# Performance work log

Measured on AMD Instinct MI355X. Metric: run time of the kernel, lower is better.

## Reference

```python
import jax, jax.numpy as jnp
import numpy as np

BN_EPS = 1e-3  # keras BatchNormalization default epsilon
NEG_INF = -1e30


def _masked_row_softmax(adjT):
    # tf.sparse.softmax semantics: softmax over NONZERO entries of each row;
    # implicit zeros stay exactly zero.
    mask = adjT != 0
    logits = jnp.where(mask, adjT, NEG_INF)
    p = jax.nn.softmax(logits, axis=-1)
    return jnp.where(mask, p, 0.0)


def _batch_norm(x, gamma, beta):
    # training-mode BN over all axes except channels
    mean = jnp.mean(x, axis=(0, 1), keepdims=True)
    var = jnp.var(x, axis=(0, 1), keepdims=True)
    return (x - mean) * jax.lax.rsqrt(var + BN_EPS) * gamma + beta


def setup_inputs() -> dict:
    key = jax.random.key(0)
    ks = jax.random.split(key, 4)
    B, N, F = 1, 8192, 128
    C0, C1 = 256, 128
    features = jax.random.normal(ks[0], (B, N, F), dtype=jnp.float32)
    adj = jax.random.randint(ks[1], (B, N, N), 0, 2, dtype=jnp.int32)
    kernel_1 = jax.random.normal(ks[2], (F, C0), dtype=jnp.float32) * (1.0 / np.sqrt(F))
    kernel_2 = jax.random.normal(ks[3], (C0, C1), dtype=jnp.float32) * (1.0 / np.sqrt(C0))
    return {
        "features": features,
        "adj": adj,
        "kernel_1": kernel_1,
        "bias_1": jnp.zeros((C0,), jnp.float32),
        "gamma_1": jnp.ones((C0,), jnp.float32),
        "beta_1": jnp.zeros((C0,), jnp.float32),
        "kernel_2": kernel_2,
        "bias_2": jnp.zeros((C1,), jnp.float32),
        "gamma_2": jnp.ones((C1,), jnp.float32),
        "beta_2": jnp.zeros((C1,), jnp.float32),
    }


def reference(features, adj, kernel_1, bias_1, gamma_1, beta_1,
              kernel_2, bias_2, gamma_2, beta_2):
    # fltr transposed: (B, Nr, Np), then sparse softmax over last dim
    adjT = jnp.transpose(adj.astype(jnp.float32), (0, 2, 1))
    w = _masked_row_softmax(adjT)                      # (B, Nr, Np)
    # people -> region aggregation + projection
    region = jnp.matmul(w, features)                   # (B, Nr, F)
    region = jnp.matmul(region, kernel_1) + bias_1     # (B, Nr, C0)
    region = _batch_norm(region, gamma_1, beta_1)
    # region -> people aggregation + projection
    people = jnp.matmul(jnp.transpose(w, (0, 2, 1)), region)  # (B, Np, C0)
    people = jnp.matmul(people, kernel_2) + bias_2             # (B, Np, C1)
    people = _batch_norm(people, gamma_2, beta_2)
    return people
```

## Files before the change

### kernel.cpp

```cpp
#include <hip/hip_runtime.h>
#include <stdint.h>

typedef unsigned int u32;
typedef unsigned short u16;
typedef __attribute__((ext_vector_type(8))) short short8;
typedef __attribute__((ext_vector_type(4))) float f32x4;

#define N8K 8192

__device__ __forceinline__ float b2f(u16 u) { return __uint_as_float(((u32)u) << 16); }
__device__ __forceinline__ u16 f2b(float f) {
  u32 i = __float_as_uint(f);
  i += 0x7FFFu + ((i >> 16) & 1u);
  return (u16)(i >> 16);
}
__device__ __forceinline__ u32 pk01(int x, int y) { return (u32)__mul24(x | (y << 16), 0x3F80); }
__device__ __forceinline__ u32 pkf(float a, float b) { return (u32)f2b(a) | ((u32)f2b(b) << 16); }

__device__ __forceinline__ int dvote(const u16* f16) {
  u16 u = f16[threadIdx.x * 2];
  int e = (u >> 7) & 0xFF;
  return __syncthreads_count((e >= 0x60 && e <= 0x9F) ? 1 : 0) >= 128;
}

__device__ __forceinline__ void gl_lds16(const void* g, void* l) {
  __builtin_amdgcn_global_load_lds(
      (const __attribute__((address_space(1))) u32*)g,
      (__attribute__((address_space(3))) u32*)l, 16, 0, 0);
}

#define MFMA_4x4(As_, Bs_, aoff_, boff_)                                         \
  {                                                                              \
    short8 afr[4], bfr[4];                                                       \
    _Pragma("unroll") for (int i_ = 0; i_ < 4; ++i_)                             \
      afr[i_] = *(const short8*)(As_ + aoff_[i_]);                               \
    _Pragma("unroll") for (int j_ = 0; j_ < 4; ++j_)                             \
      bfr[j_] = *(const short8*)(Bs_ + boff_[j_]);                               \
    _Pragma("unroll") for (int i_ = 0; i_ < 4; ++i_)                             \
      _Pragma("unroll") for (int j_ = 0; j_ < 4; ++j_)                           \
        acc[i_][j_] = __builtin_amdgcn_mfma_f32_16x16x32_bf16(                   \
            afr[i_], bfr[j_], acc[i_][j_], 0, 0, 0);                             \
  }

#define ZERO_ACC()                                                               \
  f32x4 acc[4][4];                                                               \
  {                                                                              \
    const f32x4 fz = {0.f, 0.f, 0.f, 0.f};                                       \
    _Pragma("unroll") for (int i_ = 0; i_ < 4; ++i_)                             \
      _Pragma("unroll") for (int j_ = 0; j_ < 4; ++j_) acc[i_][j_] = fz;         \
  }

__global__ void k_prep(const void* __restrict__ featv, const void* __restrict__ K1v,
                       const void* __restrict__ K2v,
                       const void* __restrict__ b1v, const void* __restrict__ g1v,
                       const void* __restrict__ be1v, const void* __restrict__ b2v,
                       const void* __restrict__ g2v, const void* __restrict__ be2v,
                       u16* __restrict__ Ft, u16* __restrict__ K1T, u16* __restrict__ K2T,
                       float* __restrict__ deg, float* __restrict__ par,
                       float* __restrict__ bn1s, float* __restrict__ bn1q,
                       float* __restrict__ bn2s, float* __restrict__ bn2q) {
  const int b = blockIdx.x, t = threadIdx.x;
  const int flag = dvote((const u16*)featv);
  if (b < 256) {
    __shared__ __align__(16) u16 Ls[32 * 136];
    const int pr = t >> 3, ck = t & 7;
    u16 v[16];
    if (flag) {
      const u16* s = (const u16*)featv + (size_t)(b * 32 + pr) * 128 + ck * 16;
      uint4 a = *(const uint4*)(s);
      uint4 bq = *(const uint4*)(s + 8);
      *(uint4*)&v[0] = a; *(uint4*)&v[8] = bq;
    } else {
      const float* s = (const float*)featv + (size_t)(b * 32 + pr) * 128 + ck * 16;
#pragma unroll
      for (int i = 0; i < 16; ++i) v[i] = f2b(s[i]);
    }
    *(uint4*)(Ls + pr * 136 + ck * 16) = *(uint4*)&v[0];
    *(uint4*)(Ls + pr * 136 + ck * 16 + 8) = *(uint4*)&v[8];
    __syncthreads();
    const int f = t >> 1, h16 = (t & 1) * 16;
    u32 w[8];
#pragma unroll
    for (int i = 0; i < 8; ++i) {
      u16 lo = Ls[(h16 + 2 * i) * 136 + f];
      u16 hi = Ls[(h16 + 2 * i + 1) * 136 + f];
      w[i] = (u32)lo | ((u32)hi << 16);
    }
    u16* d = Ft + (size_t)b * 4096 + f * 32 + h16;
    *(uint4*)(d) = *(uint4*)&w[0];
    *(uint4*)(d + 8) = *(uint4*)&w[4];
  } else if (b < 272) {
    int o = ((b - 256) * 256 + t) << 3;
    int k0 = o >> 13, c = (o >> 5) & 255, kk = o & 31;
    uint4 w;
    if (flag) {
      const u16* s = (const u16*)K1v + (size_t)(k0 * 32 + kk) * 256 + c;
      w.x = (u32)s[0]    | ((u32)s[256]  << 16);
      w.y = (u32)s[512]  | ((u32)s[768]  << 16);
      w.z = (u32)s[1024] | ((u32)s[1280] << 16);
      w.w = (u32)s[1536] | ((u32)s[1792] << 16);
    } else {
      const float* s = (const float*)K1v + (size_t)(k0 * 32 + kk) * 256 + c;
      w.x = pkf(s[0], s[256]); w.y = pkf(s[512], s[768]);
      w.z = pkf(s[1024], s[1280]); w.w = pkf(s[1536], s[1792]);
    }
    *(uint4*)(K1T + o) = w;
  } else if (b < 288) {
    int o = ((b - 272) * 256 + t) << 3;
    int k0 = o >> 12, c = (o >> 5) & 127, kk = o & 31;
    uint4 w;
    if (flag) {
      const u16* s = (const u16*)K2v + (size_t)(k0 * 32 + kk) * 128 + c;
      w.x = (u32)s[0]   | ((u32)s[128] << 16);
      w.y = (u32)s[256] | ((u32)s[384] << 16);
      w.z = (u32)s[512] | ((u32)s[640] << 16);
      w.w = (u32)s[768] | ((u32)s[896] << 16);
    } else {
      const float* s = (const float*)K2v + (size_t)(k0 * 32 + kk) * 128 + c;
      w.x = pkf(s[0], s[128]); w.y = pkf(s[256], s[384]);
      w.z = pkf(s[512], s[640]); w.w = pkf(s[768], s[896]);
    }
    *(uint4*)(K2T + o) = w;
  } else {
    if (t < 256) {
      par[t]       = flag ? b2f(((const u16*)b1v)[t])  : ((const float*)b1v)[t];
      par[256 + t] = flag ? b2f(((const u16*)g1v)[t])  : ((const float*)g1v)[t];
      par[512 + t] = flag ? b2f(((const u16*)be1v)[t]) : ((const float*)be1v)[t];
      bn1s[t] = 0.f; bn1q[t] = 0.f;
    }
    if (t < 128) {
      par[768 + t]  = flag ? b2f(((const u16*)b2v)[t])  : ((const float*)b2v)[t];
      par[896 + t]  = flag ? b2f(((const u16*)g2v)[t])  : ((const float*)g2v)[t];
      par[1024 + t] = flag ? b2f(((const u16*)be2v)[t]) : ((const float*)be2v)[t];
      bn2s[t] = 0.f; bn2q[t] = 0.f;
    }
    for (int i = t; i < N8K; i += 256) deg[i] = 0.f;
  }
}

__global__ __launch_bounds__(256, 2)
void k_gemm1(const int* __restrict__ adj, const u16* __restrict__ Ft,
             float* __restrict__ P1, float* __restrict__ deg, int ksteps) {
  __shared__ __align__(16) u16 As[128 * 32];
  __shared__ __align__(16) u16 Bs[128 * 32];
  __shared__ float degp[128];
  const int t = threadIdx.x, bx = blockIdx.x;
  const int nt = bx & 63, s = bx >> 6;
  const int n0 = nt << 7;
  const int lane = t & 63, wv = t >> 6;
  const int wm = (wv & 1) << 6, wn = (wv >> 1) << 6;
  const int fm = lane & 15, fq = lane >> 4;
  if (t < 128) degp[t] = 0.0f;
  ZERO_ACC();
  int aoff[4], boff[4];
#pragma unroll
  for (int i = 0; i < 4; ++i) aoff[i] = (wm + i * 16 + fm) * 32 + fq * 8;
#pragma unroll
  for (int j = 0; j < 4; ++j) {
    int n = wn + j * 16 + fm;
    boff[j] = n * 32 + ((fq * 8) ^ (((n >> 2) & 3) << 3));
  }
  const int rb = t & 31, kb = t >> 5;
  const int* gB = adj + ((size_t)s * ksteps * 32 + kb * 4) * N8K + n0 + rb * 4;
  const char* gA = (const char*)(Ft + (size_t)s * ksteps * 4096);
  char* lA = (char*)As + ((t >> 6) << 10);
  const int goff = t << 4;
  u16* lb = Bs + (rb * 4) * 32 + ((kb * 4) ^ ((rb & 3) << 3));
  int ds0 = 0, ds1 = 0, ds2 = 0, ds3 = 0;
  for (int ks = 0; ks < ksteps; ++ks) {
    __syncthreads();
    gl_lds16(gA + goff, lA);
    gl_lds16(gA + 4096 + goff, lA + 4096);
    int4 a0 = *(const int4*)(gB);
    int4 a1 = *(const int4*)(gB + N8K);
    int4 a2 = *(const int4*)(gB + 2 * N8K);
    int4 a3 = *(const int4*)(gB + 3 * N8K);
    gA += 8192;
    gB += 32 * N8K;
    ds0 += a0.x + a1.x + a2.x + a3.x;
    ds1 += a0.y + a1.y + a2.y + a3.y;
    ds2 += a0.z + a1.z + a2.z + a3.z;
    ds3 += a0.w + a1.w + a2.w + a3.w;
    uint2 w;
    w.x = pk01(a0.x, a1.x); w.y = pk01(a2.x, a3.x); *(uint2*)(lb) = w;
    w.x = pk01(a0.y, a1.y); w.y = pk01(a2.y, a3.y); *(uint2*)(lb + 32) = w;
    w.x = pk01(a0.z, a1.z); w.y = pk01(a2.z, a3.z); *(uint2*)(lb + 64) = w;
    w.x = pk01(a0.w, a1.w); w.y = pk01(a2.w, a3.w); *(uint2*)(lb + 96) = w;
    __syncthreads();
    MFMA_4x4(As, Bs, aoff, boff);
  }
  atomicAdd(&degp[rb * 4 + 0], (float)ds0);
  atomicAdd(&degp[rb * 4 + 1], (float)ds1);
  atomicAdd(&degp[rb * 4 + 2], (float)ds2);
  atomicAdd(&degp[rb * 4 + 3], (float)ds3);
  float* base = P1 + ((size_t)s * N8K + n0) * 128;
#pragma unroll
  for (int i = 0; i < 4; ++i)
#pragma unroll
    for (int j = 0; j < 4; ++j) {
      int r = wn + j * 16 + fm;
      int f = wm + i * 16 + fq * 4;
      *(f32x4*)(base + (size_t)r * 128 + f) = acc[i][j];
    }
  __syncthreads();
  if (t < 128) atomicAdd(&deg[n0 + t], degp[t]);
}

__global__ __launch_bounds__(256, 2)
void k_projf(const float* __restrict__ Psrc, const float* __restrict__ deg,
             const u16* __restrict__ Bt, const float* __restrict__ bias,
             float* __restrict__ Cout, float* __restrict__ bns, float* __restrict__ bnq,
             int nsplit, int ksteps, int Ncols, int useinv) {
  __shared__ __align__(16) u16 As[128 * 32];
  __shared__ __align__(16) u16 Bs[128 * 32];
  const int t = threadIdx.x, bx = blockIdx.x;
  const int ct = bx & 1, mt = (bx >> 1) & 63;
  const int m0 = mt << 7, n0 = ct << 7;
  const int lane = t & 63, wv = t >> 6;
  const int wm = (wv & 1) << 6, wn = (wv >> 1) << 6;
  const int fm = lane & 15, fq = lane >> 4;
  const int K = ksteps << 5;
  ZERO_ACC();
  int aoff[4], boff[4];
#pragma unroll
  for (int i = 0; i < 4; ++i) {
    int m = wm + i * 16 + fm;
    aoff[i] = m * 32 + ((fq * 8) ^ (((m >> 2) & 3) << 3));
  }
#pragma unroll
  for (int j = 0; j < 4; ++j) boff[j] = (wn + j * 16 + fm) * 32 + fq * 8;
  const int row = t >> 1;
  const size_t sstride = (size_t)N8K * K;
  const float* src = Psrc + (size_t)(m0 + row) * K + (t & 1) * 16;
  float inv = 1.0f;
  if (useinv) {
    float d = deg[m0 + row];
    inv = (d > 0.5f) ? 1.0f / d : 0.0f;
  }
  const int swzA = ((t >> 3) & 3) << 3;
  u16* la0 = As + row * 32 + (((t & 1) * 16) ^ swzA);
  u16* la1 = As + row * 32 + ((((t & 1) * 16) + 8) ^ swzA);
  char* lB = (char*)Bs + ((t >> 6) << 10);
  const int goff = t << 4;
  for (int ks = 0; ks < ksteps; ++ks) {
    __syncthreads();
    const char* gB = (const char*)(Bt + ((size_t)ks * Ncols + n0) * 32);
    gl_lds16(gB + goff, lB);
    gl_lds16(gB + 4096 + goff, lB + 4096);
    f32x4 s0 = {0.f, 0.f, 0.f, 0.f}, s1 = s0, s2 = s0, s3 = s0;
    const float* p = src + ks * 32;
    for (int sp = 0; sp < nsplit; ++sp) {
      const f32x4* q = (const f32x4*)(p + sp * sstride);
      s0 += q[0]; s1 += q[1]; s2 += q[2]; s3 += q[3];
    }
    s0 *= inv; s1 *= inv; s2 *= inv; s3 *= inv;
    uint4 w;
    w.x = pkf(s0[0], s0[1]); w.y = pkf(s0[2], s0[3]);
    w.z = pkf(s1[0], s1[1]); w.w = pkf(s1[2], s1[3]);
    *(uint4*)la0 = w;
    w.x = pkf(s2[0], s2[1]); w.y = pkf(s2[2], s2[3]);
    w.z = pkf(s3[0], s3[1]); w.w = pkf(s3[2], s3[3]);
    *(uint4*)la1 = w;
    __syncthreads();
    MFMA_4x4(As, Bs, aoff, boff);
  }
#pragma unroll
  for (int j = 0; j < 4; ++j) {
    int c = n0 + wn + j * 16 + fm;
    float bc = bias[c];
    float t1 = 0.f, t2 = 0.f;
#pragma unroll
    for (int i = 0; i < 4; ++i) {
      int r = m0 + wm + i * 16 + fq * 4;
#pragma unroll
      for (int ii = 0; ii < 4; ++ii) {
        float v = acc[i][j][ii] + bc;
        Cout[(size_t)(r + ii) * Ncols + c] = v;
        t1 += v; t2 += v * v;
      }
    }
    t1 += __shfl_xor(t1, 16); t1 += __shfl_xor(t1, 32);
    t2 += __shfl_xor(t2, 16); t2 += __shfl_xor(t2, 32);
    if (fq == 0) { atomicAdd(&bns[c], t1); atomicAdd(&bnq[c], t2); }
  }
}

__global__ __launch_bounds__(256, 2)
void k_bnH(const float* __restrict__ region1, const float* __restrict__ deg,
           const float* __restrict__ bn1s, const float* __restrict__ bn1q,
           const float* __restrict__ g1, const float* __restrict__ be1,
           const u16* __restrict__ K2T, u16* __restrict__ HT) {
  __shared__ __align__(16) u16 As[128 * 32];
  __shared__ __align__(16) u16 Bs[128 * 32];
  __shared__ float scS[256], shS[256];
  const int t = threadIdx.x, mt = blockIdx.x;
  const int m0 = mt << 7;
  const int lane = t & 63, wv = t >> 6;
  const int wm = (wv & 1) << 6, wn = (wv >> 1) << 6;
  const int fm = lane & 15, fq = lane >> 4;
  {
    float mu = bn1s[t] * (1.0f / 8192.0f);
    float var = bn1q[t] * (1.0f / 8192.0f) - mu * mu;
    float iv = rsqrtf(var + 1e-3f);
    float sc = iv * g1[t];
    scS[t] = sc;
    shS[t] = be1[t] - mu * sc;
  }
  ZERO_ACC();
  int aoff[4], boff[4];
#pragma unroll
  for (int i = 0; i < 4; ++i) {
    int m = wm + i * 16 + fm;
    aoff[i] = m * 32 + ((fq * 8) ^ (((m >> 2) & 3) << 3));
  }
#pragma unroll
  for (int j = 0; j < 4; ++j) boff[j] = (wn + j * 16 + fm) * 32 + fq * 8;
  const int row = t >> 1, half = t & 1;
  float d = deg[m0 + row];
  const float idg = (d > 0.5f) ? 1.0f / d : 0.0f;
  const float* src = region1 + (size_t)(m0 + row) * 256 + half * 16;
  const int swzA = ((t >> 3) & 3) << 3;
  u16* la0 = As + row * 32 + ((half * 16) ^ swzA);
  u16* la1 = As + row * 32 + (((half * 16) + 8) ^ swzA);
  char* lB = (char*)Bs + ((t >> 6) << 10);
  const int goff = t << 4;
  for (int ks = 0; ks < 8; ++ks) {
    __syncthreads();
    const char* gB = (const char*)(K2T + (size_t)ks * 4096);
    gl_lds16(gB + goff, lB);
    gl_lds16(gB + 4096 + goff, lB + 4096);
    const float* p = src + ks * 32;
    const int cb = ks * 32 + half * 16;
    float y[16];
#pragma unroll
    for (int q = 0; q < 4; ++q) {
      f32x4 x = *(const f32x4*)(p + q * 4);
#pragma unroll
      for (int jj = 0; jj < 4; ++jj)
        y[q * 4 + jj] = (x[jj] * scS[cb + q * 4 + jj] + shS[cb + q * 4 + jj]) * idg;
    }
    uint4 w;
    w.x = pkf(y[0], y[1]); w.y = pkf(y[2], y[3]);
    w.z = pkf(y[4], y[5]); w.w = pkf(y[6], y[7]);
    *(uint4*)la0 = w;
    w.x = pkf(y[8], y[9]); w.y = pkf(y[10], y[11]);
    w.z = pkf(y[12], y[13]); w.w = pkf(y[14], y[15]);
    *(uint4*)la1 = w;
    __syncthreads();
    MFMA_4x4(As, Bs, aoff, boff);
  }
#pragma unroll
  for (int i = 0; i < 4; ++i)
#pragma unroll
    for (int j = 0; j < 4; ++j) {
      int c = wn + j * 16 + fm;
      int r = m0 + wm + i * 16 + fq * 4;
      uint2 w;
      w.x = pkf(acc[i][j][0], acc[i][j][1]);
      w.y = pkf(acc[i][j][2], acc[i][j][3]);
      *(uint2*)(HT + (size_t)(r >> 5) * 4096 + c * 32 + (r & 31)) = w;
    }
}

__global__ __launch_bounds__(256, 2)
void k_gemm2(const int* __restrict__ adj, const u16* __restrict__ HT,
             float* __restrict__ P2, int ksteps) {
  __shared__ __align__(16) u16 As[128 * 32];
  __shared__ __align__(16) u16 Bs[128 * 32];
  const int t = threadIdx.x, bx = blockIdx.x;
  const int mt = bx & 63, s = bx >> 6;
  const int m0 = mt << 7;
  const int lane = t & 63, wv = t >> 6;
  const int wm = (wv & 1) << 6, wn = (wv >> 1) << 6;
  const int fm = lane & 15, fq = lane >> 4;
  ZERO_ACC();
  int aoff[4], boff[4];
#pragma unroll
  for (int i = 0; i < 4; ++i) {
    int m = wm + i * 16 + fm;
    aoff[i] = m * 32 + ((fq * 8) ^ (((m >> 2) & 3) << 3));
  }
#pragma unroll
  for (int j = 0; j < 4; ++j) boff[j] = (wn + j * 16 + fm) * 32 + fq * 8;
  const int row = t >> 1, half = t & 1;
  const int* gA = adj + (size_t)(m0 + row) * N8K + (size_t)s * ksteps * 32 + half * 16;
  const char* gB = (const char*)(HT + (size_t)s * ksteps * 4096);
  char* lB = (char*)Bs + ((t >> 6) << 10);
  const int goff = t << 4;
  const int swzA = ((t >> 3) & 3) << 3;
  u16* la0 = As + row * 32 + ((half * 16) ^ swzA);
  u16* la1 = As + row * 32 + (((half * 16) + 8) ^ swzA);
  for (int ks = 0; ks < ksteps; ++ks) {
    __syncthreads();
    gl_lds16(gB + goff, lB);
    gl_lds16(gB + 4096 + goff, lB + 4096);
    int4 a0 = *(const int4*)(gA);
    int4 a1 = *(const int4*)(gA + 4);
    int4 a2 = *(const int4*)(gA + 8);
    int4 a3 = *(const int4*)(gA + 12);
    gA += 32;
    gB += 8192;
    uint4 w;
    w.x = pk01(a0.x, a0.y); w.y = pk01(a0.z, a0.w);
    w.z = pk01(a1.x, a1.y); w.w = pk01(a1.z, a1.w);
    *(uint4*)la0 = w;
    w.x = pk01(a2.x, a2.y); w.y = pk01(a2.z, a2.w);
    w.z = pk01(a3.x, a3.y); w.w = pk01(a3.z, a3.w);
    *(uint4*)la1 = w;
    __syncthreads();
    MFMA_4x4(As, Bs, aoff, boff);
  }
  float* base = P2 + (size_t)s * N8K * 128;
#pragma unroll
  for (int i = 0; i < 4; ++i)
#pragma unroll
    for (int j = 0; j < 4; ++j) {
      int c = wn + j * 16 + fm;
      int pr = m0 + wm + i * 16 + fq * 4;
#pragma unroll
      for (int ii = 0; ii < 4; ++ii)
        base[(size_t)(pr + ii) * 128 + c] = acc[i][j][ii];
    }
}

__global__ void k_red2(const float* __restrict__ P2, const float* __restrict__ bias,
                       float* __restrict__ people1,
                       float* __restrict__ bn2s, float* __restrict__ bn2q) {
  __shared__ float r1[256], r2[256];
  const int t = threadIdx.x;
  const int c = t & 127, pg = t >> 7;
  const int p0 = blockIdx.x << 5;
  const float bc = bias[c];
  float s1 = 0.f, s2 = 0.f;
  for (int pp = pg; pp < 32; pp += 2) {
    size_t o = (size_t)(p0 + pp) * 128 + c;
    float v = bc;
#pragma unroll
    for (int s = 0; s < 8; ++s) v += P2[(size_t)s * N8K * 128 + o];
    people1[o] = v;
    s1 += v; s2 += v * v;
  }
  r1[t] = s1; r2[t] = s2;
  __syncthreads();
  if (t < 128) {
    atomicAdd(&bn2s[t], r1[t] + r1[t + 128]);
    atomicAdd(&bn2q[t], r2[t] + r2[t + 128]);
  }
}

__global__ void k_bn2apply(const float* __restrict__ people1,
                           const float* __restrict__ bn2s, const float* __restrict__ bn2q,
                           const float* __restrict__ g2, const float* __restrict__ be2,
                           const u16* __restrict__ featprobe, void* __restrict__ outv) {
  const int flag = dvote(featprobe);
  int g = blockIdx.x * 256 + threadIdx.x;
  int p = g >> 5;
  int c = (g & 31) << 2;
  f32x4 x = *(const f32x4*)(people1 + (size_t)p * 128 + c);
  f32x4 y;
#pragma unroll
  for (int jj = 0; jj < 4; ++jj) {
    int cc = c + jj;
    float mu = bn2s[cc] * (1.0f / 8192.0f);
    float var = bn2q[cc] * (1.0f / 8192.0f) - mu * mu;
    float inv = rsqrtf(var + 1e-3f);
    y[jj] = (x[jj] - mu) * inv * g2[cc] + be2[cc];
  }
  if (flag) {
    uint2 w;
    w.x = pkf(y[0], y[1]);
    w.y = pkf(y[2], y[3]);
    *(uint2*)((u16*)outv + (size_t)p * 128 + c) = w;
  } else {
    *(f32x4*)((float*)outv + (size_t)p * 128 + c) = y;
  }
}

extern "C" void kernel_launch(void* const* d_in, const int* in_sizes, int n_in,
                              void* d_out, int out_size, void* d_ws, size_t ws_size,
                              hipStream_t stream) {
  const void* feat = d_in[0];
  const int* adj   = (const int*)d_in[1];
  const void* K1   = d_in[2];
  const void* b1   = d_in[3];
  const void* g1   = d_in[4];
  const void* be1  = d_in[5];
  const void* K2   = d_in[6];
  const void* b2   = d_in[7];
  const void* g2   = d_in[8];
  const void* be2  = d_in[9];
  char* ws = (char*)d_ws;
  const size_t MB = 1u << 20;

  float* Pbig    = (float*)(ws);
  float* region1 = (float*)(ws + 32 * MB);
  float* people1 = (float*)(ws + 40 * MB);
  u16*   Ft      = (u16*)(ws + 44 * MB);
  u16*   HT      = (u16*)(ws + 46 * MB);
  u16*   K1T     = (u16*)(ws + 48 * MB);
  u16*   K2T     = K1T + 32768;
  float* deg     = (float*)(K2T + 32768);
  float* par     = deg + N8K;
  float* bn1s    = par + 1152;
  float* bn1q    = bn1s + 256;
  float* bn2s    = bn1q + 256;
  float* bn2q    = bn2s + 128;

  k_prep<<<289, 256, 0, stream>>>(feat, K1, K2, b1, g1, be1, b2, g2, be2,
                                  Ft, K1T, K2T, deg, par, bn1s, bn1q, bn2s, bn2q);
  k_gemm1<<<512, 256, 0, stream>>>(adj, Ft, Pbig, deg, 32);
  k_projf<<<128, 256, 0, stream>>>(Pbig, deg, K1T, par + 0, region1, bn1s, bn1q,
                                   8, 4, 256, 1);
  k_bnH<<<64, 256, 0, stream>>>(region1, deg, bn1s, bn1q, par + 256, par + 512,
                                K2T, HT);
  k_gemm2<<<512, 256, 0, stream>>>(adj, HT, Pbig, 32);
  k_red2<<<256, 256, 0, stream>>>(Pbig, par + 768, people1, bn2s, bn2q);
  k_bn2apply<<<1024, 256, 0, stream>>>(people1, bn2s, bn2q, par + 896, par + 1024,
                                       (const u16*)feat, d_out);
}
```

Baseline: 497.6 us.

## Pre-pack adjacency into row and column bitmasks shared by both GEMMs

A new pass in the prep kernel reads the 256 MB int32 adjacency once and writes two compact bitmasks: one row-major and one transposed, each 8 MB. Both GEMMs then read 32-bit mask words instead of int4 loads and expand the bits to bf16 0/1 in LDS. GEMM1 counts degrees with popcount. This replaces two full passes over the int32 adjacency with one pass plus small bitmask reads. In exchange, prep now launches about 16K blocks and does LDS transposes with per-row and per-column ballots.

```diff
diff --git a/kernel.cpp b/kernel.cpp
--- a/kernel.cpp
+++ b/kernel.cpp
@@ -3,6 +3,7 @@
 
 typedef unsigned int u32;
 typedef unsigned short u16;
+typedef unsigned long long u64;
 typedef __attribute__((ext_vector_type(8))) short short8;
 typedef __attribute__((ext_vector_type(4))) float f32x4;
 
@@ -14,7 +15,6 @@
   i += 0x7FFFu + ((i >> 16) & 1u);
   return (u16)(i >> 16);
 }
-__device__ __forceinline__ u32 pk01(int x, int y) { return (u32)__mul24(x | (y << 16), 0x3F80); }
 __device__ __forceinline__ u32 pkf(float a, float b) { return (u32)f2b(a) | ((u32)f2b(b) << 16); }
 
 __device__ __forceinline__ int dvote(const u16* f16) {
@@ -27,6 +27,17 @@
   __builtin_amdgcn_global_load_lds(
       (const __attribute__((address_space(1))) u32*)g,
       (__attribute__((address_space(3))) u32*)l, 16, 0, 0);
+}
+
+__device__ __forceinline__ void unpack16(u32 b, uint4& o0, uint4& o1) {
+  o0.x = ((b & 0x0001u) ? 0x3F80u : 0u) | ((b & 0x0002u) ? 0x3F800000u : 0u);
+  o0.y = ((b & 0x0004u) ? 0x3F80u : 0u) | ((b & 0x0008u) ? 0x3F800000u : 0u);
+  o0.z = ((b & 0x0010u) ? 0x3F80u : 0u) | ((b & 0x0020u) ? 0x3F800000u : 0u);
+  o0.w = ((b & 0x0040u) ? 0x3F80u : 0u) | ((b & 0x0080u) ? 0x3F800000u : 0u);
+  o1.x = ((b & 0x0100u) ? 0x3F80u : 0u) | ((b & 0x0200u) ? 0x3F800000u : 0u);
+  o1.y = ((b & 0x0400u) ? 0x3F80u : 0u) | ((b & 0x0800u) ? 0x3F800000u : 0u);
+  o1.z = ((b & 0x1000u) ? 0x3F80u : 0u) | ((b & 0x2000u) ? 0x3F800000u : 0u);
+  o1.w = ((b & 0x4000u) ? 0x3F80u : 0u) | ((b & 0x8000u) ? 0x3F800000u : 0u);
 }
 
 #define MFMA_4x4(As_, Bs_, aoff_, boff_)                                         \
@@ -50,47 +61,75 @@
       _Pragma("unroll") for (int j_ = 0; j_ < 4; ++j_) acc[i_][j_] = fz;         \
   }
 
-__global__ void k_prep(const void* __restrict__ featv, const void* __restrict__ K1v,
+__global__ void k_prep(const int* __restrict__ adj,
+                       const void* __restrict__ featv, const void* __restrict__ K1v,
                        const void* __restrict__ K2v,
                        const void* __restrict__ b1v, const void* __restrict__ g1v,
                        const void* __restrict__ be1v, const void* __restrict__ b2v,
                        const void* __restrict__ g2v, const void* __restrict__ be2v,
+                       u32* __restrict__ RB, u32* __restrict__ CB,
                        u16* __restrict__ Ft, u16* __restrict__ K1T, u16* __restrict__ K2T,
                        float* __restrict__ deg, float* __restrict__ par,
                        float* __restrict__ bn1s, float* __restrict__ bn1q,
                        float* __restrict__ bn2s, float* __restrict__ bn2q) {
+  __shared__ u32 Ls[64 * 65];
+  __shared__ __align__(16) u16 Lf[32 * 136];
   const int b = blockIdx.x, t = threadIdx.x;
-  const int flag = dvote((const u16*)featv);
-  if (b < 256) {
-    __shared__ __align__(16) u16 Ls[32 * 136];
+  if (b < 16384) {
+    const int r0 = (b & 127) << 6, p0 = (b >> 7) << 6;
+    const int lr = t >> 4, lc = (t & 15) << 2;
+#pragma unroll
+    for (int k = 0; k < 4; ++k) {
+      int row = k * 16 + lr;
+      int4 v = *(const int4*)(adj + (size_t)(p0 + row) * N8K + r0 + lc);
+      u32* d = &Ls[row * 65 + lc];
+      d[0] = (u32)v.x; d[1] = (u32)v.y; d[2] = (u32)v.z; d[3] = (u32)v.w;
+    }
+    __syncthreads();
+    const int wv = t >> 6, l = t & 63;
+#pragma unroll 4
+    for (int i = 0; i < 16; ++i) {
+      int row = wv * 16 + i;
+      u64 m = __ballot(Ls[row * 65 + l] != 0u);
+      if (l == 0) *(u64*)(RB + (size_t)(p0 + row) * 256 + (r0 >> 5)) = m;
+    }
+#pragma unroll 4
+    for (int i = 0; i < 16; ++i) {
+      int col = wv * 16 + i;
+      u64 m = __ballot(Ls[l * 65 + col] != 0u);
+      if (l == 0) *(u64*)(CB + (size_t)(r0 + col) * 256 + (p0 >> 5)) = m;
+    }
+  } else if (b < 16640) {
+    const int flag = dvote((const u16*)featv);
+    const int bb = b - 16384;
     const int pr = t >> 3, ck = t & 7;
     u16 v[16];
     if (flag) {
-      const u16* s = (const u16*)featv + (size_t)(b * 32 + pr) * 128 + ck * 16;
-      uint4 a = *(const uint4*)(s);
-      uint4 bq = *(const uint4*)(s + 8);
-      *(uint4*)&v[0] = a; *(uint4*)&v[8] = bq;
+      const u16* s = (const u16*)featv + (size_t)(bb * 32 + pr) * 128 + ck * 16;
+      *(uint4*)&v[0] = *(const uint4*)(s);
+      *(uint4*)&v[8] = *(const uint4*)(s + 8);
     } else {
-      const float* s = (const float*)featv + (size_t)(b * 32 + pr) * 128 + ck * 16;
+      const float* s = (const float*)featv + (size_t)(bb * 32 + pr) * 128 + ck * 16;
 #pragma unroll
       for (int i = 0; i < 16; ++i) v[i] = f2b(s[i]);
     }
-    *(uint4*)(Ls + pr * 136 + ck * 16) = *(uint4*)&v[0];
-    *(uint4*)(Ls + pr * 136 + ck * 16 + 8) = *(uint4*)&v[8];
+    *(uint4*)(Lf + pr * 136 + ck * 16) = *(uint4*)&v[0];
+    *(uint4*)(Lf + pr * 136 + ck * 16 + 8) = *(uint4*)&v[8];
     __syncthreads();
     const int f = t >> 1, h16 = (t & 1) * 16;
     u32 w[8];
 #pragma unroll
     for (int i = 0; i < 8; ++i) {
-      u16 lo = Ls[(h16 + 2 * i) * 136 + f];
-      u16 hi = Ls[(h16 + 2 * i + 1) * 136 + f];
+      u16 lo = Lf[(h16 + 2 * i) * 136 + f];
+      u16 hi = Lf[(h16 + 2 * i + 1) * 136 + f];
       w[i] = (u32)lo | ((u32)hi << 16);
     }
-    u16* d = Ft + (size_t)b * 4096 + f * 32 + h16;
+    u16* d = Ft + (size_t)bb * 4096 + f * 32 + h16;
     *(uint4*)(d) = *(uint4*)&w[0];
     *(uint4*)(d + 8) = *(uint4*)&w[4];
-  } else if (b < 272) {
-    int o = ((b - 256) * 256 + t) << 3;
+  } else if (b < 16656) {
+    const int flag = dvote((const u16*)featv);
+    int o = ((b - 16640) * 256 + t) << 3;
     int k0 = o >> 13, c = (o >> 5) & 255, kk = o & 31;
     uint4 w;
     if (flag) {
@@ -105,8 +144,9 @@
       w.z = pkf(s[1024], s[1280]); w.w = pkf(s[1536], s[1792]);
     }
     *(uint4*)(K1T + o) = w;
-  } else if (b < 288) {
-    int o = ((b - 272) * 256 + t) << 3;
+  } else if (b < 16672) {
+    const int flag = dvote((const u16*)featv);
+    int o = ((b - 16656) * 256 + t) << 3;
     int k0 = o >> 12, c = (o >> 5) & 127, kk = o & 31;
     uint4 w;
     if (flag) {
@@ -122,6 +162,7 @@
     }
     *(uint4*)(K2T + o) = w;
   } else {
+    const int flag = dvote((const u16*)featv);
     if (t < 256) {
       par[t]       = flag ? b2f(((const u16*)b1v)[t])  : ((const float*)b1v)[t];
       par[256 + t] = flag ? b2f(((const u16*)g1v)[t])  : ((const float*)g1v)[t];
@@ -139,7 +180,7 @@
 }
 
 __global__ __launch_bounds__(256, 2)
-void k_gemm1(const int* __restrict__ adj, const u16* __restrict__ Ft,
+void k_gemm1(const u32* __restrict__ CB, const u16* __restrict__ Ft,
              float* __restrict__ P1, float* __restrict__ deg, int ksteps) {
   __shared__ __align__(16) u16 As[128 * 32];
   __shared__ __align__(16) u16 Bs[128 * 32];
@@ -160,39 +201,31 @@
     int n = wn + j * 16 + fm;
     boff[j] = n * 32 + ((fq * 8) ^ (((n >> 2) & 3) << 3));
   }
-  const int rb = t & 31, kb = t >> 5;
-  const int* gB = adj + ((size_t)s * ksteps * 32 + kb * 4) * N8K + n0 + rb * 4;
+  const int row = t >> 1, h = t & 1;
+  const u32* gB = CB + (size_t)(n0 + row) * 256 + s * ksteps;
   const char* gA = (const char*)(Ft + (size_t)s * ksteps * 4096);
   char* lA = (char*)As + ((t >> 6) << 10);
   const int goff = t << 4;
-  u16* lb = Bs + (rb * 4) * 32 + ((kb * 4) ^ ((rb & 3) << 3));
-  int ds0 = 0, ds1 = 0, ds2 = 0, ds3 = 0;
+  const int swz = ((row >> 2) & 3) << 3;
+  u16* lb0 = Bs + row * 32 + ((h * 16) ^ swz);
+  u16* lb1 = Bs + row * 32 + (((h * 16) + 8) ^ swz);
+  int cnt = 0;
   for (int ks = 0; ks < ksteps; ++ks) {
     __syncthreads();
     gl_lds16(gA + goff, lA);
     gl_lds16(gA + 4096 + goff, lA + 4096);
-    int4 a0 = *(const int4*)(gB);
-    int4 a1 = *(const int4*)(gB + N8K);
-    int4 a2 = *(const int4*)(gB + 2 * N8K);
-    int4 a3 = *(const int4*)(gB + 3 * N8K);
+    u32 w = gB[ks];
     gA += 8192;
-    gB += 32 * N8K;
-    ds0 += a0.x + a1.x + a2.x + a3.x;
-    ds1 += a0.y + a1.y + a2.y + a3.y;
-    ds2 += a0.z + a1.z + a2.z + a3.z;
-    ds3 += a0.w + a1.w + a2.w + a3.w;
-    uint2 w;
-    w.x = pk01(a0.x, a1.x); w.y = pk01(a2.x, a3.x); *(uint2*)(lb) = w;
-    w.x = pk01(a0.y, a1.y); w.y = pk01(a2.y, a3.y); *(uint2*)(lb + 32) = w;
-    w.x = pk01(a0.z, a1.z); w.y = pk01(a2.z, a3.z); *(uint2*)(lb + 64) = w;
-    w.x = pk01(a0.w, a1.w); w.y = pk01(a2.w, a3.w); *(uint2*)(lb + 96) = w;
+    u32 bits = (w >> (h * 16)) & 0xFFFFu;
+    cnt += __popc(bits);
+    uint4 o0, o1;
+    unpack16(bits, o0, o1);
+    *(uint4*)lb0 = o0;
+    *(uint4*)lb1 = o1;
     __syncthreads();
     MFMA_4x4(As, Bs, aoff, boff);
   }
-  atomicAdd(&degp[rb * 4 + 0], (float)ds0);
-  atomicAdd(&degp[rb * 4 + 1], (float)ds1);
-  atomicAdd(&degp[rb * 4 + 2], (float)ds2);
-  atomicAdd(&degp[rb * 4 + 3], (float)ds3);
+  atomicAdd(&degp[row], (float)cnt);
   float* base = P1 + ((size_t)s * N8K + n0) * 128;
 #pragma unroll
   for (int i = 0; i < 4; ++i)
@@ -363,7 +396,7 @@
 }
 
 __global__ __launch_bounds__(256, 2)
-void k_gemm2(const int* __restrict__ adj, const u16* __restrict__ HT,
+void k_gemm2(const u32* __restrict__ RB, const u16* __restrict__ HT,
              float* __restrict__ P2, int ksteps) {
   __shared__ __align__(16) u16 As[128 * 32];
   __shared__ __align__(16) u16 Bs[128 * 32];
@@ -382,31 +415,25 @@
   }
 #pragma unroll
   for (int j = 0; j < 4; ++j) boff[j] = (wn + j * 16 + fm) * 32 + fq * 8;
-  const int row = t >> 1, half = t & 1;
-  const int* gA = adj + (size_t)(m0 + row) * N8K + (size_t)s * ksteps * 32 + half * 16;
+  const int row = t >> 1, h = t & 1;
+  const u32* gA = RB + (size_t)(m0 + row) * 256 + s * ksteps;
   const char* gB = (const char*)(HT + (size_t)s * ksteps * 4096);
   char* lB = (char*)Bs + ((t >> 6) << 10);
   const int goff = t << 4;
-  const int swzA = ((t >> 3) & 3) << 3;
-  u16* la0 = As + row * 32 + ((half * 16) ^ swzA);
-  u16* la1 = As + row * 32 + (((half * 16) + 8) ^ swzA);
+  const int swzA = ((row >> 2) & 3) << 3;
+  u16* la0 = As + row * 32 + ((h * 16) ^ swzA);
+  u16* la1 = As + row * 32 + (((h * 16) + 8) ^ swzA);
   for (int ks = 0; ks < ksteps; ++ks) {
     __syncthreads();
     gl_lds16(gB + goff, lB);
     gl_lds16(gB + 4096 + goff, lB + 4096);
-    int4 a0 = *(const int4*)(gA);
-    int4 a1 = *(const int4*)(gA + 4);
-    int4 a2 = *(const int4*)(gA + 8);
-    int4 a3 = *(const int4*)(gA + 12);
-    gA += 32;
+    u32 w = gA[ks];
     gB += 8192;
-    uint4 w;
-    w.x = pk01(a0.x, a0.y); w.y = pk01(a0.z, a0.w);
-    w.z = pk01(a1.x, a1.y); w.w = pk01(a1.z, a1.w);
-    *(uint4*)la0 = w;
-    w.x = pk01(a2.x, a2.y); w.y = pk01(a2.z, a2.w);
-    w.z = pk01(a3.x, a3.y); w.w = pk01(a3.z, a3.w);
-    *(uint4*)la1 = w;
+    u32 bits = (w >> (h * 16)) & 0xFFFFu;
+    uint4 o0, o1;
+    unpack16(bits, o0, o1);
+    *(uint4*)la0 = o0;
+    *(uint4*)la1 = o1;
     __syncthreads();
     MFMA_4x4(As, Bs, aoff, boff);
   }
@@ -497,7 +524,9 @@
   float* people1 = (float*)(ws + 40 * MB);
   u16*   Ft      = (u16*)(ws + 44 * MB);
   u16*   HT      = (u16*)(ws + 46 * MB);
-  u16*   K1T     = (u16*)(ws + 48 * MB);
+  u32*   RB      = (u32*)(ws + 48 * MB);
+  u32*   CB      = (u32*)(ws + 56 * MB);
+  u16*   K1T     = (u16*)(ws + 64 * MB);
   u16*   K2T     = K1T + 32768;
   float* deg     = (float*)(K2T + 32768);
   float* par     = deg + N8K;
@@ -506,14 +535,15 @@
   float* bn2s    = bn1q + 256;
   float* bn2q    = bn2s + 128;
 
-  k_prep<<<289, 256, 0, stream>>>(feat, K1, K2, b1, g1, be1, b2, g2, be2,
-                                  Ft, K1T, K2T, deg, par, bn1s, bn1q, bn2s, bn2q);
-  k_gemm1<<<512, 256, 0, stream>>>(adj, Ft, Pbig, deg, 32);
+  k_prep<<<16673, 256, 0, stream>>>(adj, feat, K1, K2, b1, g1, be1, b2, g2, be2,
+                                    RB, CB, Ft, K1T, K2T, deg, par,
+                                    bn1s, bn1q, bn2s, bn2q);
+  k_gemm1<<<512, 256, 0, stream>>>(CB, Ft, Pbig, deg, 32);
   k_projf<<<128, 256, 0, stream>>>(Pbig, deg, K1T, par + 0, region1, bn1s, bn1q,
                                    8, 4, 256, 1);
   k_bnH<<<64, 256, 0, stream>>>(region1, deg, bn1s, bn1q, par + 256, par + 512,
                                 K2T, HT);
-  k_gemm2<<<512, 256, 0, stream>>>(adj, HT, Pbig, 32);
+  k_gemm2<<<512, 256, 0, stream>>>(RB, HT, Pbig, 32);
   k_red2<<<256, 256, 0, stream>>>(Pbig, par + 768, people1, bn2s, bn2q);
   k_bn2apply<<<1024, 256, 0, stream>>>(people1, bn2s, bn2q, par + 896, par + 1024,
                                        (const u16*)feat, d_out);
```

New measurement: 508.1 us. +2.1%, slower.

## Pack adjacency into bitmask during first GEMM and reuse it in second GEMM

Applied to the files above, without the earlier changes.

The first aggregation GEMM now also packs each 0/1 int32 adjacency entry into a bit, combining lanes with wave shuffles and writing a compact 8 MB bitmask to workspace. The second GEMM reads this bitmask instead of re-reading the 256 MB int32 adjacency matrix. It expands the bits to bf16 ones and zeros in registers before storing them to LDS. This removes most of the second full pass over the adjacency at the cost of extra shuffles and stores in the first GEMM. It assumes adjacency values are strictly 0 or 1.

```diff
diff --git a/kernel.cpp b/kernel.cpp
--- a/kernel.cpp
+++ b/kernel.cpp
@@ -3,6 +3,7 @@
 
 typedef unsigned int u32;
 typedef unsigned short u16;
+typedef unsigned long long u64;
 typedef __attribute__((ext_vector_type(8))) short short8;
 typedef __attribute__((ext_vector_type(4))) float f32x4;
 
@@ -27,6 +28,17 @@
   __builtin_amdgcn_global_load_lds(
       (const __attribute__((address_space(1))) u32*)g,
       (__attribute__((address_space(3))) u32*)l, 16, 0, 0);
+}
+
+__device__ __forceinline__ void unpack16(u32 b, uint4& o0, uint4& o1) {
+  o0.x = ((b & 0x0001u) ? 0x3F80u : 0u) | ((b & 0x0002u) ? 0x3F800000u : 0u);
+  o0.y = ((b & 0x0004u) ? 0x3F80u : 0u) | ((b & 0x0008u) ? 0x3F800000u : 0u);
+  o0.z = ((b & 0x0010u) ? 0x3F80u : 0u) | ((b & 0x0020u) ? 0x3F800000u : 0u);
+  o0.w = ((b & 0x0040u) ? 0x3F80u : 0u) | ((b & 0x0080u) ? 0x3F800000u : 0u);
+  o1.x = ((b & 0x0100u) ? 0x3F80u : 0u) | ((b & 0x0200u) ? 0x3F800000u : 0u);
+  o1.y = ((b & 0x0400u) ? 0x3F80u : 0u) | ((b & 0x0800u) ? 0x3F800000u : 0u);
+  o1.z = ((b & 0x1000u) ? 0x3F80u : 0u) | ((b & 0x2000u) ? 0x3F800000u : 0u);
+  o1.w = ((b & 0x4000u) ? 0x3F80u : 0u) | ((b & 0x8000u) ? 0x3F800000u : 0u);
 }
 
 #define MFMA_4x4(As_, Bs_, aoff_, boff_)                                         \
@@ -62,28 +74,27 @@
   const int b = blockIdx.x, t = threadIdx.x;
   const int flag = dvote((const u16*)featv);
   if (b < 256) {
-    __shared__ __align__(16) u16 Ls[32 * 136];
+    __shared__ __align__(16) u16 Lf[32 * 136];
     const int pr = t >> 3, ck = t & 7;
     u16 v[16];
     if (flag) {
       const u16* s = (const u16*)featv + (size_t)(b * 32 + pr) * 128 + ck * 16;
-      uint4 a = *(const uint4*)(s);
-      uint4 bq = *(const uint4*)(s + 8);
-      *(uint4*)&v[0] = a; *(uint4*)&v[8] = bq;
+      *(uint4*)&v[0] = *(const uint4*)(s);
+      *(uint4*)&v[8] = *(const uint4*)(s + 8);
     } else {
       const float* s = (const float*)featv + (size_t)(b * 32 + pr) * 128 + ck * 16;
 #pragma unroll
       for (int i = 0; i < 16; ++i) v[i] = f2b(s[i]);
     }
-    *(uint4*)(Ls + pr * 136 + ck * 16) = *(uint4*)&v[0];
-    *(uint4*)(Ls + pr * 136 + ck * 16 + 8) = *(uint4*)&v[8];
+    *(uint4*)(Lf + pr * 136 + ck * 16) = *(uint4*)&v[0];
+    *(uint4*)(Lf + pr * 136 + ck * 16 + 8) = *(uint4*)&v[8];
     __syncthreads();
     const int f = t >> 1, h16 = (t & 1) * 16;
     u32 w[8];
 #pragma unroll
     for (int i = 0; i < 8; ++i) {
-      u16 lo = Ls[(h16 + 2 * i) * 136 + f];
-      u16 hi = Ls[(h16 + 2 * i + 1) * 136 + f];
+      u16 lo = Lf[(h16 + 2 * i) * 136 + f];
+      u16 hi = Lf[(h16 + 2 * i + 1) * 136 + f];
       w[i] = (u32)lo | ((u32)hi << 16);
     }
     u16* d = Ft + (size_t)b * 4096 + f * 32 + h16;
@@ -140,7 +151,8 @@
 
 __global__ __launch_bounds__(256, 2)
 void k_gemm1(const int* __restrict__ adj, const u16* __restrict__ Ft,
-             float* __restrict__ P1, float* __restrict__ deg, int ksteps) {
+             float* __restrict__ P1, float* __restrict__ deg,
+             u32* __restrict__ RB, int ksteps) {
   __shared__ __align__(16) u16 As[128 * 32];
   __shared__ __align__(16) u16 Bs[128 * 32];
   __shared__ float degp[128];
@@ -166,6 +178,9 @@
   char* lA = (char*)As + ((t >> 6) << 10);
   const int goff = t << 4;
   u16* lb = Bs + (rb * 4) * 32 + ((kb * 4) ^ ((rb & 3) << 3));
+  const int sh4 = (rb & 7) * 4;
+  const int rbw = (n0 >> 5) + (rb >> 3);
+  const int pb0 = s * ksteps * 32 + kb * 4;
   int ds0 = 0, ds1 = 0, ds2 = 0, ds3 = 0;
   for (int ks = 0; ks < ksteps; ++ks) {
     __syncthreads();
@@ -186,6 +201,18 @@
     w.x = pk01(a0.y, a1.y); w.y = pk01(a2.y, a3.y); *(uint2*)(lb + 32) = w;
     w.x = pk01(a0.z, a1.z); w.y = pk01(a2.z, a3.z); *(uint2*)(lb + 64) = w;
     w.x = pk01(a0.w, a1.w); w.y = pk01(a2.w, a3.w); *(uint2*)(lb + 96) = w;
+    u32 v0 = ((u32)a0.x | ((u32)a0.y << 1) | ((u32)a0.z << 2) | ((u32)a0.w << 3)) << sh4;
+    u32 v1 = ((u32)a1.x | ((u32)a1.y << 1) | ((u32)a1.z << 2) | ((u32)a1.w << 3)) << sh4;
+    u32 v2 = ((u32)a2.x | ((u32)a2.y << 1) | ((u32)a2.z << 2) | ((u32)a2.w << 3)) << sh4;
+    u32 v3 = ((u32)a3.x | ((u32)a3.y << 1) | ((u32)a3.z << 2) | ((u32)a3.w << 3)) << sh4;
+    v0 |= __shfl_xor(v0, 1); v0 |= __shfl_xor(v0, 2); v0 |= __shfl_xor(v0, 4);
+    v1 |= __shfl_xor(v1, 1); v1 |= __shfl_xor(v1, 2); v1 |= __shfl_xor(v1, 4);
+    v2 |= __shfl_xor(v2, 1); v2 |= __shfl_xor(v2, 2); v2 |= __shfl_xor(v2, 4);
+    v3 |= __shfl_xor(v3, 1); v3 |= __shfl_xor(v3, 2); v3 |= __shfl_xor(v3, 4);
+    if ((rb & 7) == 0) {
+      u32* dst = RB + (size_t)(pb0 + ks * 32) * 256 + rbw;
+      dst[0] = v0; dst[256] = v1; dst[512] = v2; dst[768] = v3;
+    }
     __syncthreads();
     MFMA_4x4(As, Bs, aoff, boff);
   }
@@ -363,7 +390,7 @@
 }
 
 __global__ __launch_bounds__(256, 2)
-void k_gemm2(const int* __restrict__ adj, const u16* __restrict__ HT,
+void k_gemm2(const u32* __restrict__ RB, const u16* __restrict__ HT,
              float* __restrict__ P2, int ksteps) {
   __shared__ __align__(16) u16 As[128 * 32];
   __shared__ __align__(16) u16 Bs[128 * 32];
@@ -382,31 +409,25 @@
   }
 #pragma unroll
   for (int j = 0; j < 4; ++j) boff[j] = (wn + j * 16 + fm) * 32 + fq * 8;
-  const int row = t >> 1, half = t & 1;
-  const int* gA = adj + (size_t)(m0 + row) * N8K + (size_t)s * ksteps * 32 + half * 16;
+  const int row = t >> 1, h = t & 1;
+  const u32* gA = RB + (size_t)(m0 + row) * 256 + s * ksteps;
   const char* gB = (const char*)(HT + (size_t)s * ksteps * 4096);
   char* lB = (char*)Bs + ((t >> 6) << 10);
   const int goff = t << 4;
-  const int swzA = ((t >> 3) & 3) << 3;
-  u16* la0 = As + row * 32 + ((half * 16) ^ swzA);
-  u16* la1 = As + row * 32 + (((half * 16) + 8) ^ swzA);
+  const int swzA = ((row >> 2) & 3) << 3;
+  u16* la0 = As + row * 32 + ((h * 16) ^ swzA);
+  u16* la1 = As + row * 32 + (((h * 16) + 8) ^ swzA);
   for (int ks = 0; ks < ksteps; ++ks) {
     __syncthreads();
     gl_lds16(gB + goff, lB);
     gl_lds16(gB + 4096 + goff, lB + 4096);
-    int4 a0 = *(const int4*)(gA);
-    int4 a1 = *(const int4*)(gA + 4);
-    int4 a2 = *(const int4*)(gA + 8);
-    int4 a3 = *(const int4*)(gA + 12);
-    gA += 32;
+    u32 w = gA[ks];
     gB += 8192;
-    uint4 w;
-    w.x = pk01(a0.x, a0.y); w.y = pk01(a0.z, a0.w);
-    w.z = pk01(a1.x, a1.y); w.w = pk01(a1.z, a1.w);
-    *(uint4*)la0 = w;
-    w.x = pk01(a2.x, a2.y); w.y = pk01(a2.z, a2.w);
-    w.z = pk01(a3.x, a3.y); w.w = pk01(a3.z, a3.w);
-    *(uint4*)la1 = w;
+    u32 bits = (w >> (h * 16)) & 0xFFFFu;
+    uint4 o0, o1;
+    unpack16(bits, o0, o1);
+    *(uint4*)la0 = o0;
+    *(uint4*)la1 = o1;
     __syncthreads();
     MFMA_4x4(As, Bs, aoff, boff);
   }
@@ -497,7 +518,8 @@
   float* people1 = (float*)(ws + 40 * MB);
   u16*   Ft      = (u16*)(ws + 44 * MB);
   u16*   HT      = (u16*)(ws + 46 * MB);
-  u16*   K1T     = (u16*)(ws + 48 * MB);
+  u32*   RB      = (u32*)(ws + 48 * MB);
+  u16*   K1T     = (u16*)(ws + 56 * MB);
   u16*   K2T     = K1T + 32768;
   float* deg     = (float*)(K2T + 32768);
   float* par     = deg + N8K;
@@ -508,12 +530,12 @@
 
   k_prep<<<289, 256, 0, stream>>>(feat, K1, K2, b1, g1, be1, b2, g2, be2,
                                   Ft, K1T, K2T, deg, par, bn1s, bn1q, bn2s, bn2q);
-  k_gemm1<<<512, 256, 0, stream>>>(adj, Ft, Pbig, deg, 32);
+  k_gemm1<<<512, 256, 0, stream>>>(adj, Ft, Pbig, deg, RB, 32);
   k_projf<<<128, 256, 0, stream>>>(Pbig, deg, K1T, par + 0, region1, bn1s, bn1q,
                                    8, 4, 256, 1);
   k_bnH<<<64, 256, 0, stream>>>(region1, deg, bn1s, bn1q, par + 256, par + 512,
                                 K2T, HT);
-  k_gemm2<<<512, 256, 0, stream>>>(adj, HT, Pbig, 32);
+  k_gemm2<<<512, 256, 0, stream>>>(RB, HT, Pbig, 32);
   k_red2<<<256, 256, 0, stream>>>(Pbig, par + 768, people1, bn2s, bn2q);
   k_bn2apply<<<1024, 256, 0, stream>>>(people1, bn2s, bn2q, par + 896, par + 1024,
                                        (const u16*)feat, d_out);
```

Measured after the change: 480.8 us. -3.4%, faster.
